# Performance work log

Hardware: AMD Instinct MI355X
Metric: run time of the kernel (lower is better)

## Reference

```python
import jax, jax.numpy as jnp
import numpy as np


def setup_inputs() -> dict:
    key = jax.random.key(0)
    k1, k2 = jax.random.split(key)
    batch = jax.random.normal(k1, (16, 256, 1024), dtype=jnp.float32)
    # probe matrix initialized uniform(-0.05, 0.05) as in the original
    B = jax.random.uniform(k2, (1024, 128), minval=-0.05, maxval=0.05, dtype=jnp.float32)
    return {"batch": batch, "B": B}


def reference(batch, B):
    # project: (b, s, d) @ (d, r) -> (b, s, r)
    transformed = jnp.einsum("bsd,dr->bsr", batch, B)
    # pairwise squared L2 distances via broadcast: (b, s, 1, r) - (b, 1, s, r)
    diffs = transformed[:, :, None, :] - transformed[:, None, :, :]
    # (b, s, s)
    return jnp.sum(diffs * diffs, axis=-1)
```

## Files before the change

kernel.cpp:

```cpp
#include <hip/hip_runtime.h>
#include <hip/hip_bf16.h>

typedef __bf16 bf16x8 __attribute__((ext_vector_type(8)));
typedef float f32x4 __attribute__((ext_vector_type(4)));

#define K_DIM 1024
#define N_DIM 128


__device__ inline unsigned pk2(float x, float y) {
  __hip_bfloat16 hx = __float2bfloat16(x), hy = __float2bfloat16(y);
  return (unsigned)*(unsigned short*)&hx | ((unsigned)*(unsigned short*)&hy << 16);
}

__global__ __launch_bounds__(64)
void prep_kernel(const float* __restrict__ B, unsigned short* __restrict__ Bfrag) {
  const int W = blockIdx.x, l = threadIdx.x;
  const int w = W >> 5, ks = W & 31;
  const int col = 16 * w + (l & 15);
  const int kb = 32 * ks + 4 * (l >> 4);
  unsigned u[4];
#pragma unroll
  for (int j = 0; j < 4; ++j) {
    int k0 = kb + 2 * (j & 1) + 16 * (j >> 1);
    u[j] = pk2(B[(size_t)k0 * N_DIM + col], B[(size_t)(k0 + 1) * N_DIM + col]);
  }
  *(uint4*)&Bfrag[((size_t)(w * 32 + ks) * 64 + l) * 8] =
      make_uint4(u[0], u[1], u[2], u[3]);
}

__global__ __launch_bounds__(512, 2)
void proj_kernel(const float* __restrict__ batch,
                 const unsigned short* __restrict__ Bfrag,
                 unsigned short* __restrict__ Tfrag, float* __restrict__ nrm) {
  __shared__ __align__(16) unsigned short Asl[32 * 64 * 8];
  __shared__ float part[8][16];
  const int t = threadIdx.x, w = t >> 6, l = t & 63;
  const int blk = blockIdx.x;
  const int m0 = blk * 16;

  {
    const float* src = batch + (size_t)m0 * K_DIM;
#pragma unroll
    for (int j = 0; j < 8; ++j) {
      int fidx = j * 512 + t;
      f32x4 v = *(const f32x4*)(src + 4 * (size_t)fidx);
      int r = fidx >> 8;
      int q = fidx & 255;
      int ks = q >> 3, qq = q & 7, g = qq & 3, h = qq >> 2;
      int byte = ks * 1024 + ((16 * (r + 16 * g)) ^ ((ks & 7) << 4)) + 8 * h;
      *(uint2*)((char*)Asl + byte) = make_uint2(pk2(v.x, v.y), pk2(v.z, v.w));
    }
  }

  bf16x8 bfr[32];
  {
    const unsigned short* bptr = Bfrag + ((size_t)w * 32 * 64 + l) * 8;
#pragma unroll
    for (int ks = 0; ks < 32; ++ks)
      bfr[ks] = *(const bf16x8*)(bptr + (size_t)ks * 512);
  }
  __syncthreads();

  f32x4 acc0 = {0.f, 0.f, 0.f, 0.f}, acc1 = {0.f, 0.f, 0.f, 0.f};
#pragma unroll
  for (int ks = 0; ks < 32; ks += 2) {
    bf16x8 a0 = *(const bf16x8*)((const char*)Asl +
                   (ks * 1024 + ((l * 16) ^ ((ks & 7) << 4))));
    acc0 = __builtin_amdgcn_mfma_f32_16x16x32_bf16(bfr[ks], a0, acc0, 0, 0, 0);
    bf16x8 a1 = *(const bf16x8*)((const char*)Asl +
                   ((ks + 1) * 1024 + ((l * 16) ^ (((ks + 1) & 7) << 4))));
    acc1 = __builtin_amdgcn_mfma_f32_16x16x32_bf16(bfr[ks + 1], a1, acc1, 0, 0, 0);
  }
  f32x4 acc = acc0 + acc1;

  unsigned lo = pk2(acc[0], acc[1]);
  unsigned hi = pk2(acc[2], acc[3]);
  *(uint2*)&Tfrag[(((size_t)blk * 4 + (w >> 1)) * 64 + l) * 8 + (w & 1) * 4] =
      make_uint2(lo, hi);

  float v0 = __uint_as_float(lo << 16);
  float v1 = __uint_as_float(lo & 0xffff0000u);
  float v2 = __uint_as_float(hi << 16);
  float v3 = __uint_as_float(hi & 0xffff0000u);
  float s = v0 * v0 + v1 * v1 + v2 * v2 + v3 * v3;
  s += __shfl_xor(s, 16);
  s += __shfl_xor(s, 32);
  if (l < 16) part[w][l] = s;
  __syncthreads();
  if (t < 16) {
    float n = 0.f;
#pragma unroll
    for (int ww = 0; ww < 8; ++ww) n += part[ww][t];
    nrm[m0 + t] = n;
  }
}

__global__ __launch_bounds__(256)
void dist_kernel(const unsigned short* __restrict__ Tfrag,
                 const float* __restrict__ nrm, float* __restrict__ out) {
  const int t = threadIdx.x, l = t & 63;
  const int W = blockIdx.x * 4 + (t >> 6);
  const int bb = W >> 8, tile = W & 255;
  const int ti = (tile >> 4) * 16, tj = (tile & 15) * 16;
  const int rbase = bb * 256;

  bf16x8 ifr[4], jfr[4];
#pragma unroll
  for (int ks = 0; ks < 4; ++ks) {
    ifr[ks] = *(const bf16x8*)
        &Tfrag[((((size_t)bb * 16 + (ti >> 4)) * 4 + ks) * 64 + l) * 8];
    jfr[ks] = *(const bf16x8*)
        &Tfrag[((((size_t)bb * 16 + (tj >> 4)) * 4 + ks) * 64 + l) * 8];
  }

  f32x4 acc = {0.f, 0.f, 0.f, 0.f};
#pragma unroll
  for (int ks = 0; ks < 4; ++ks)
    acc = __builtin_amdgcn_mfma_f32_16x16x32_bf16(ifr[ks], jfr[ks], acc, 0, 0, 0);

  const float njv = nrm[rbase + tj + (l & 15)];
  const f32x4 ni = *(const f32x4*)&nrm[rbase + ti + 4 * (l >> 4)];
#pragma unroll
  for (int ii = 0; ii < 4; ++ii) {
    out[(size_t)(rbase + ti + 4 * (l >> 4) + ii) * 256 + tj + (l & 15)] =
        ni[ii] + njv - 2.f * acc[ii];
  }
}

extern "C" void kernel_launch(void* const* d_in, const int* in_sizes, int n_in,
                              void* d_out, int out_size, void* d_ws, size_t ws_size,
                              hipStream_t stream) {
  const float* batch = (const float*)d_in[0];
  const float* Bmat  = (const float*)d_in[1];
  unsigned short* Bfrag = (unsigned short*)d_ws;
  unsigned short* Tfrag = Bfrag + 8 * 32 * 64 * 8;
  float* nrm = (float*)(Tfrag + 256 * 4 * 64 * 8);
  float* out = (float*)d_out;

  prep_kernel<<<256, 64, 0, stream>>>(Bmat, Bfrag);
  proj_kernel<<<256, 512, 0, stream>>>(batch, Bfrag, Tfrag, nrm);
  dist_kernel<<<1024, 256, 0, stream>>>(Tfrag, nrm, out);
}
```

Measured before the change: 20.52 us.

## Recompute row norms in dist kernel from bf16 fragments and drop norm buffer

The projection kernel no longer computes squared norms. That removes its second barrier, its shared partial array and the global norm writes. The distance kernel now rebuilds both row norms from the bf16 fragments it already holds, using per-lane sums of squares plus cross-lane shuffles. The batch staging loop is also rewritten so each thread does two 16-byte loads and one 16-byte shared store per fragment, replacing many 8-byte stores. The price is redundant norm computation in every distance tile and more shuffles in the epilogue.

```diff
diff --git a/kernel.cpp b/kernel.cpp
--- a/kernel.cpp
+++ b/kernel.cpp
@@ -32,9 +32,8 @@
 __global__ __launch_bounds__(512, 2)
 void proj_kernel(const float* __restrict__ batch,
                  const unsigned short* __restrict__ Bfrag,
-                 unsigned short* __restrict__ Tfrag, float* __restrict__ nrm) {
+                 unsigned short* __restrict__ Tfrag) {
   __shared__ __align__(16) unsigned short Asl[32 * 64 * 8];
-  __shared__ float part[8][16];
   const int t = threadIdx.x, w = t >> 6, l = t & 63;
   const int blk = blockIdx.x;
   const int m0 = blk * 16;
@@ -42,14 +41,17 @@
   {
     const float* src = batch + (size_t)m0 * K_DIM;
 #pragma unroll
-    for (int j = 0; j < 8; ++j) {
-      int fidx = j * 512 + t;
-      f32x4 v = *(const f32x4*)(src + 4 * (size_t)fidx);
-      int r = fidx >> 8;
-      int q = fidx & 255;
-      int ks = q >> 3, qq = q & 7, g = qq & 3, h = qq >> 2;
-      int byte = ks * 1024 + ((16 * (r + 16 * g)) ^ ((ks & 7) << 4)) + 8 * h;
-      *(uint2*)((char*)Asl + byte) = make_uint2(pk2(v.x, v.y), pk2(v.z, v.w));
+    for (int j = 0; j < 4; ++j) {
+      int f = j * 512 + t;
+      int ks = f >> 6, lane = f & 63;
+      int r = lane & 15, g = lane >> 4;
+      const float* p = src + (size_t)r * K_DIM + 32 * ks + 4 * g;
+      f32x4 g0 = *(const f32x4*)p;
+      f32x4 g1 = *(const f32x4*)(p + 16);
+      uint4 u = make_uint4(pk2(g0.x, g0.y), pk2(g0.z, g0.w),
+                           pk2(g1.x, g1.y), pk2(g1.z, g1.w));
+      int byte = ks * 1024 + ((lane * 16) ^ ((ks & 7) << 4));
+      *(uint4*)((char*)Asl + byte) = u;
     }
   }
 
@@ -74,31 +76,13 @@
   }
   f32x4 acc = acc0 + acc1;
 
-  unsigned lo = pk2(acc[0], acc[1]);
-  unsigned hi = pk2(acc[2], acc[3]);
   *(uint2*)&Tfrag[(((size_t)blk * 4 + (w >> 1)) * 64 + l) * 8 + (w & 1) * 4] =
-      make_uint2(lo, hi);
-
-  float v0 = __uint_as_float(lo << 16);
-  float v1 = __uint_as_float(lo & 0xffff0000u);
-  float v2 = __uint_as_float(hi << 16);
-  float v3 = __uint_as_float(hi & 0xffff0000u);
-  float s = v0 * v0 + v1 * v1 + v2 * v2 + v3 * v3;
-  s += __shfl_xor(s, 16);
-  s += __shfl_xor(s, 32);
-  if (l < 16) part[w][l] = s;
-  __syncthreads();
-  if (t < 16) {
-    float n = 0.f;
-#pragma unroll
-    for (int ww = 0; ww < 8; ++ww) n += part[ww][t];
-    nrm[m0 + t] = n;
-  }
+      make_uint2(pk2(acc[0], acc[1]), pk2(acc[2], acc[3]));
 }
 
 __global__ __launch_bounds__(256)
 void dist_kernel(const unsigned short* __restrict__ Tfrag,
-                 const float* __restrict__ nrm, float* __restrict__ out) {
+                 float* __restrict__ out) {
   const int t = threadIdx.x, l = t & 63;
   const int W = blockIdx.x * 4 + (t >> 6);
   const int bb = W >> 8, tile = W & 255;
@@ -119,12 +103,25 @@
   for (int ks = 0; ks < 4; ++ks)
     acc = __builtin_amdgcn_mfma_f32_16x16x32_bf16(ifr[ks], jfr[ks], acc, 0, 0, 0);
 
-  const float njv = nrm[rbase + tj + (l & 15)];
-  const f32x4 ni = *(const f32x4*)&nrm[rbase + ti + 4 * (l >> 4)];
+  float si = 0.f, sj = 0.f;
+#pragma unroll
+  for (int ks = 0; ks < 4; ++ks)
+#pragma unroll
+    for (int e = 0; e < 8; ++e) {
+      float vi = (float)ifr[ks][e];
+      float vj = (float)jfr[ks][e];
+      si += vi * vi;
+      sj += vj * vj;
+    }
+  si += __shfl_xor(si, 16); si += __shfl_xor(si, 32);
+  sj += __shfl_xor(sj, 16); sj += __shfl_xor(sj, 32);
+
 #pragma unroll
   for (int ii = 0; ii < 4; ++ii) {
-    out[(size_t)(rbase + ti + 4 * (l >> 4) + ii) * 256 + tj + (l & 15)] =
-        ni[ii] + njv - 2.f * acc[ii];
+    int row = 4 * (l >> 4) + ii;
+    float ni = __shfl(si, row);
+    out[(size_t)(rbase + ti + row) * 256 + tj + (l & 15)] =
+        ni + sj - 2.f * acc[ii];
   }
 }
 
@@ -133,12 +130,11 @@
                               hipStream_t stream) {
   const float* batch = (const float*)d_in[0];
   const float* Bmat  = (const float*)d_in[1];
-  unsigned short* Bfrag = (unsigned short*)d_ws;
-  unsigned short* Tfrag = Bfrag + 8 * 32 * 64 * 8;
-  float* nrm = (float*)(Tfrag + 256 * 4 * 64 * 8);
+  unsigned short* Tfrag = (unsigned short*)d_ws;
+  unsigned short* Bfrag = Tfrag + 256 * 4 * 64 * 8;
   float* out = (float*)d_out;
 
   prep_kernel<<<256, 64, 0, stream>>>(Bmat, Bfrag);
-  proj_kernel<<<256, 512, 0, stream>>>(batch, Bfrag, Tfrag, nrm);
-  dist_kernel<<<1024, 256, 0, stream>>>(Tfrag, nrm, out);
+  proj_kernel<<<256, 512, 0, stream>>>(batch, Bfrag, Tfrag);
+  dist_kernel<<<1024, 256, 0, stream>>>(Tfrag, out);
 }
```

After: 21.35 us. 4.0% more time.
